# Optimization experiments

Hardware: AMD Instinct MI355X
Metric: run time of the kernel (lower is better)

Reference implementation:

```python
import jax, jax.numpy as jnp
import numpy as np

CARD = [3049, 10, 7, 3]
EMB = 16
HID = 64
COV = 10
B = 4096
S = 512
IN_DIM = 1 + COV + len(CARD) * EMB + 1  # 76


def setup_inputs() -> dict:
    key = jax.random.key(0)
    ks = jax.random.split(key, 12)
    target = jax.random.uniform(ks[0], (B, S), dtype=jnp.float32) * 100.0
    covariates = jax.random.normal(ks[1], (B, S, COV), dtype=jnp.float32)
    static_cats = jax.random.randint(ks[2], (B, len(CARD)), 0, 3)
    scale = jax.random.uniform(ks[3], (B, 1), dtype=jnp.float32) * 10.0 + 0.1
    emb0 = jax.random.normal(ks[4], (CARD[0], EMB), dtype=jnp.float32) * 0.1
    emb1 = jax.random.normal(ks[5], (CARD[1], EMB), dtype=jnp.float32) * 0.1
    emb2 = jax.random.normal(ks[6], (CARD[2], EMB), dtype=jnp.float32) * 0.1
    emb3 = jax.random.normal(ks[7], (CARD[3], EMB), dtype=jnp.float32) * 0.1
    w_ih = jax.random.normal(ks[8], (IN_DIM, 4 * HID), dtype=jnp.float32) / np.sqrt(IN_DIM)
    w_hh = jax.random.normal(ks[9], (HID, 4 * HID), dtype=jnp.float32) / np.sqrt(HID)
    bias = jnp.zeros((4 * HID,), dtype=jnp.float32)
    w_out = jax.random.normal(ks[10], (HID, 2), dtype=jnp.float32) / np.sqrt(HID)
    b_out = jnp.zeros((2,), dtype=jnp.float32)
    return dict(target=target, covariates=covariates, static_cats=static_cats,
                scale=scale, emb0=emb0, emb1=emb1, emb2=emb2, emb3=emb3,
                w_ih=w_ih, w_hh=w_hh, bias=bias, w_out=w_out, b_out=b_out)


def reference(target, covariates, static_cats, scale,
              emb0, emb1, emb2, emb3, w_ih, w_hh, bias, w_out, b_out):
    # static embedding concat: [B, 4*EMB]
    static_emb = jnp.concatenate([emb0[static_cats[:, 0]], emb1[static_cats[:, 1]],
                                  emb2[static_cats[:, 2]], emb3[static_cats[:, 3]]], axis=-1)
    log_scale = jnp.log1p(scale)                              # [B, 1]
    static_x = jnp.concatenate([static_emb, log_scale], -1)  # [B, 4*EMB+1]
    # teacher-forced previous scaled target: shifted target/scale, zero at t=0
    ps = target / jnp.maximum(scale, 1e-4)                    # [B, S]
    prev = jnp.concatenate([jnp.zeros_like(ps[:, :1]), ps[:, :-1]], axis=1)

    h0 = jnp.zeros((target.shape[0], w_hh.shape[0]), dtype=target.dtype)

    def step(carry, xs):
        h, c = carry
        p_t, cov_t = xs  # [B], [B, COV]
        x = jnp.concatenate([p_t[:, None], cov_t, static_x], axis=-1)  # [B, IN_DIM]
        gates = x @ w_ih + h @ w_hh + bias
        i, f, g, o = jnp.split(gates, 4, axis=-1)
        i = jax.nn.sigmoid(i)
        f = jax.nn.sigmoid(f)
        g = jnp.tanh(g)
        o = jax.nn.sigmoid(o)
        c = f * c + i * g
        h = o * jnp.tanh(c)
        raw = h @ w_out + b_out                    # [B, 2]
        mu_s = jax.nn.softplus(raw[:, 0]) + 1e-4   # [B]
        al = jax.nn.softplus(raw[:, 1]) + 1e-4     # [B]
        return (h, c), (mu_s, al)

    xs = (prev.T, jnp.swapaxes(covariates, 0, 1))  # time-major
    _, (mu_s, al) = jax.lax.scan(step, (h0, h0), xs)
    mus = mu_s.T * scale   # [B, S]
    alphas = al.T          # [B, S]
    return mus, alphas
```

## Files before the change

### kernel.cpp

```cpp
#include <hip/hip_runtime.h>

#define BB 4096
#define SS 512
#define NG 256
#define BT 16
#define NT 512
#define CH 32
#define HSTR 68
#define PSTR 16
#define SBSTR 264
#define OSTR 33

typedef __bf16 bf16_t;
typedef bf16_t bf16x8 __attribute__((ext_vector_type(8)));
typedef float  f32x4  __attribute__((ext_vector_type(4)));

__device__ __forceinline__ unsigned short f2bf(float x) {
    union { float f; unsigned u; } q{x};
    unsigned r = (q.u + 0x7fffu + ((q.u >> 16) & 1u)) >> 16;
    return (unsigned short)r;
}
__device__ __forceinline__ float bf2f(unsigned short s) {
    union { unsigned u; float f; } q{((unsigned)s) << 16};
    return q.f;
}
#define LOG2E 1.4426950408889634f
__device__ __forceinline__ float frcp_(float x)  { return __builtin_amdgcn_rcpf(x); }
__device__ __forceinline__ float fexp2_(float x) { return __builtin_amdgcn_exp2f(x); }
__device__ __forceinline__ float flog2_(float x) { return __builtin_amdgcn_logf(x); }
__device__ __forceinline__ float softplus_(float x){ return x > 20.0f ? x : 0.6931471805599453f * flog2_(1.0f + fexp2_(LOG2E * x)); }

__global__ __launch_bounds__(NT)
void deepar_kernel(const float* __restrict__ target, const float* __restrict__ cov,
                   const int* __restrict__ cats, const float* __restrict__ scale,
                   const float* __restrict__ emb0, const float* __restrict__ emb1,
                   const float* __restrict__ emb2, const float* __restrict__ emb3,
                   const float* __restrict__ w_ih, const float* __restrict__ w_hh,
                   const float* __restrict__ bias, const float* __restrict__ w_out,
                   const float* __restrict__ b_out, float* __restrict__ out)
{
    __shared__ __attribute__((aligned(16))) unsigned char smemA[2 * CH * BT * PSTR * 2];
    __shared__ __attribute__((aligned(16))) unsigned short hbuf[2][BT][HSTR];
    __shared__ float obuf[2][CH][OSTR];
    __shared__ float inv_s[BT], scl_s[BT];

    unsigned short* pcx   = (unsigned short*)smemA;
    float*          sbias = (float*)smemA;
    float*          sx    = (float*)(smemA + BT * SBSTR * 4);

    const int tid  = threadIdx.x;
    const int b0   = blockIdx.x * BT;
    const int lane = tid & 63;
    const int wv   = tid >> 6;
    const int qd   = lane >> 4;
    const int ln   = lane & 15;
    const int wvg  = wv & 3;
    const int tid2 = tid & 255;

    for (int i = tid; i < 2 * BT * HSTR; i += NT) ((unsigned short*)hbuf)[i] = 0;
    if (tid < BT) {
        float s = scale[b0 + tid];
        scl_s[tid] = s;
        inv_s[tid] = 1.0f / fmaxf(s, 1e-4f);
        sx[tid * 68 + 64] = log1pf(s);
    }
    if (tid < BT * 4) {
        int r = tid >> 2, e = tid & 3;
        int c = cats[(b0 + r) * 4 + e];
        const float* eb = (e == 0 ? emb0 : e == 1 ? emb1 : e == 2 ? emb2 : emb3);
        for (int j = 0; j < 16; ++j) sx[r * 68 + e * 16 + j] = eb[c * 16 + j];
    }
    __syncthreads();

    {
        const int n = tid & 255, half = tid >> 8;
        float bj = bias[n];
        float acc[8];
        #pragma unroll
        for (int r = 0; r < 8; ++r) acc[r] = bj;
        for (int k = 0; k < 65; ++k) {
            float w = w_ih[(11 + k) * NG + n];
            #pragma unroll
            for (int r = 0; r < 8; ++r) acc[r] += sx[(half * 8 + r) * 68 + k] * w;
        }
        #pragma unroll
        for (int r = 0; r < 8; ++r) sbias[(half * 8 + r) * SBSTR + n] = acc[r];
    }
    __syncthreads();

    bf16x8 bfrag[4][3];
    f32x4  sbf[4];
    {
        #pragma unroll
        for (int ti = 0; ti < 4; ++ti) {
            const float gsc = (ti == 2) ? (-2.0f * LOG2E) : (-LOG2E);
            const int n = ln + 16 * (wvg + 4 * ti);
            #pragma unroll
            for (int c = 0; c < 3; ++c) {
                #pragma unroll
                for (int j = 0; j < 8; ++j) {
                    int k = qd * 8 + 32 * c + j;
                    float w;
                    if (k < 64)                  w = w_hh[k * NG + n];
                    else if (k == 64 || k == 75) w = w_ih[n];
                    else if (k <= 74)            w = w_ih[(k - 64) * NG + n];
                    else                         w = 0.0f;
                    bfrag[ti][c][j] = (bf16_t)(w * gsc);
                }
            }
            #pragma unroll
            for (int r = 0; r < 4; ++r)
                sbf[ti][r] = sbias[(qd * 4 + r) * SBSTR + n] * gsc;
        }
    }

    bf16x8 wob0, wob1;
    f32x4  bC;
    float  scl4[4];
    #pragma unroll
    for (int j = 0; j < 8; ++j) {
        wob0[j] = (bf16_t)((ln < 2) ? w_out[(qd * 8 + j) * 2 + ln] : 0.0f);
        wob1[j] = (bf16_t)((ln < 2) ? w_out[(32 + qd * 8 + j) * 2 + ln] : 0.0f);
    }
    #pragma unroll
    for (int r = 0; r < 4; ++r) {
        bC[r]   = (ln < 2) ? b_out[ln] : 0.0f;
        scl4[r] = (ln == 0) ? scl_s[qd * 4 + r] : 1.0f;
    }

    __syncthreads();

    for (int i = tid; i < (2 * CH * BT * PSTR) / 2; i += NT) ((int*)smemA)[i] = 0;
    __syncthreads();

    if (tid < 256) {
        const int row = tid >> 4, i5 = tid & 15;
        const float* cr = cov + (size_t)(b0 + row) * (SS * 10);
        #pragma unroll
        for (int j = 0; j < 20; ++j) {
            int e = i5 + 16 * j, tp = e / 10, k = e - 10 * tp;
            pcx[((0 * CH + tp) * BT + row) * PSTR + 1 + k] = f2bf(cr[e]);
        }
        float pv0 = (i5 == 0) ? 0.0f : target[(size_t)(b0 + row) * SS + i5 - 1] * inv_s[row];
        float pv1 = target[(size_t)(b0 + row) * SS + i5 + 15] * inv_s[row];
        unsigned short m0 = f2bf(pv0), m1 = f2bf(pv1);
        pcx[((0 * CH + i5) * BT + row) * PSTR + 0]       = m0;
        pcx[((0 * CH + i5) * BT + row) * PSTR + 11]      = f2bf(pv0 - bf2f(m0));
        pcx[((0 * CH + i5 + 16) * BT + row) * PSTR + 0]  = m1;
        pcx[((0 * CH + i5 + 16) * BT + row) * PSTR + 11] = f2bf(pv1 - bf2f(m1));
    }
    __syncthreads();

    bf16x8 a2 = {};
    f32x4 acc_pre[4];
    {
        if (qd < 2)
            a2 = *(const bf16x8*)&pcx[((0 * CH + 0) * BT + ln) * PSTR + qd * 8];
        #pragma unroll
        for (int ti = 0; ti < 4; ++ti)
            acc_pre[ti] = __builtin_amdgcn_mfma_f32_16x16x32_bf16(a2, bfrag[ti][2], sbf[ti], 0, 0, 0);
    }

    float cst[2] = {0.0f, 0.0f};
    float crg[20];
    #pragma unroll
    for (int j = 0; j < 20; ++j) crg[j] = 0.0f;
    float trg0 = 0.0f, trg1 = 0.0f;

#define CELL(CI, RI)                                                            \
    {                                                                           \
        float si = frcp_(1.0f + fexp2_(acc0[RI]));                              \
        float sf = frcp_(1.0f + fexp2_(acc1[RI]));                              \
        float tg = 2.0f * frcp_(1.0f + fexp2_(acc2[RI])) - 1.0f;                \
        float so = frcp_(1.0f + fexp2_(acc3[RI]));                              \
        float cc = sf * cst[CI] + si * tg;                                      \
        cst[CI] = cc;                                                           \
        float th = 2.0f * frcp_(1.0f + fexp2_((-2.0f * LOG2E) * cc)) - 1.0f;    \
        *(bf16_t*)&hbuf[nxt][qd * 4 + RI][u] = (bf16_t)(so * th);               \
    }

    for (int t = 0; t < SS; ++t) {
        const int cur = t & 1, nxt = cur ^ 1;
        __syncthreads();

        const unsigned short* hb = &hbuf[cur][ln][0];
        bf16x8 a0 = *(const bf16x8*)(hb + qd * 8);
        bf16x8 a1 = *(const bf16x8*)(hb + 32 + qd * 8);

        f32x4 acc0 = __builtin_amdgcn_mfma_f32_16x16x32_bf16(a0, bfrag[0][0], acc_pre[0], 0, 0, 0);
        f32x4 acc1 = __builtin_amdgcn_mfma_f32_16x16x32_bf16(a0, bfrag[1][0], acc_pre[1], 0, 0, 0);
        f32x4 acc2 = __builtin_amdgcn_mfma_f32_16x16x32_bf16(a0, bfrag[2][0], acc_pre[2], 0, 0, 0);
        f32x4 acc3 = __builtin_amdgcn_mfma_f32_16x16x32_bf16(a0, bfrag[3][0], acc_pre[3], 0, 0, 0);
        acc0 = __builtin_amdgcn_mfma_f32_16x16x32_bf16(a1, bfrag[0][1], acc0, 0, 0, 0);
        acc1 = __builtin_amdgcn_mfma_f32_16x16x32_bf16(a1, bfrag[1][1], acc1, 0, 0, 0);
        acc2 = __builtin_amdgcn_mfma_f32_16x16x32_bf16(a1, bfrag[2][1], acc2, 0, 0, 0);
        acc3 = __builtin_amdgcn_mfma_f32_16x16x32_bf16(a1, bfrag[3][1], acc3, 0, 0, 0);

        if (t + 1 < SS && qd < 2)
            a2 = *(const bf16x8*)&pcx[((((t + 1) >> 5) & 1) * CH + ((t + 1) & 31)) * BT * PSTR
                                      + ln * PSTR + qd * 8];

        const int u = 16 * wvg + ln;
        if (wv < 4) { CELL(0, 0); CELL(1, 1); }
        else        { CELL(0, 2); CELL(1, 3); }

        if (t > 0 && wv == (t & 7)) {
            f32x4 hacc = __builtin_amdgcn_mfma_f32_16x16x32_bf16(a0, wob0, bC, 0, 0, 0);
            hacc = __builtin_amdgcn_mfma_f32_16x16x32_bf16(a1, wob1, hacc, 0, 0, 0);
            if (ln < 2) {
                #pragma unroll
                for (int r = 0; r < 4; ++r) {
                    float sp = softplus_(hacc[r]) + 1e-4f;
                    obuf[((t - 1) >> 5) & 1][(t - 1) & 31][ln * 16 + qd * 4 + r] = sp * scl4[r];
                }
            }
        }

        if (t + 1 < SS) {
            #pragma unroll
            for (int ti = 0; ti < 4; ++ti)
                acc_pre[ti] = __builtin_amdgcn_mfma_f32_16x16x32_bf16(a2, bfrag[ti][2], sbf[ti], 0, 0, 0);
        }

        if (wv >= 4) {
            if ((t & 31) == 0 && t < 480) {
                const int row = tid2 >> 4, i5 = tid2 & 15, t0n = t + CH;
                const float* cr = cov + (size_t)(b0 + row) * (SS * 10) + t0n * 10;
                #pragma unroll
                for (int j = 0; j < 20; ++j) crg[j] = cr[i5 + 16 * j];
                const float* tr = target + (size_t)(b0 + row) * SS + t0n + i5;
                trg0 = tr[-1];
                trg1 = tr[15];
            }

            if ((t & 31) == 16) {
                const int c = t >> 5;
                if (c < 15) {
                    const int row = tid2 >> 4, i5 = tid2 & 15, nb = (c + 1) & 1;
                    float pv0 = trg0 * inv_s[row];
                    float pv1 = trg1 * inv_s[row];
                    unsigned short m0 = f2bf(pv0), m1 = f2bf(pv1);
                    pcx[((nb * CH + i5) * BT + row) * PSTR + 0]       = m0;
                    pcx[((nb * CH + i5) * BT + row) * PSTR + 11]      = f2bf(pv0 - bf2f(m0));
                    pcx[((nb * CH + i5 + 16) * BT + row) * PSTR + 0]  = m1;
                    pcx[((nb * CH + i5 + 16) * BT + row) * PSTR + 11] = f2bf(pv1 - bf2f(m1));
                    #pragma unroll
                    for (int j = 0; j < 20; ++j) {
                        int e = i5 + 16 * j, tp = e / 10, k = e - 10 * tp;
                        pcx[((nb * CH + tp) * BT + row) * PSTR + 1 + k] = f2bf(crg[j]);
                    }
                }
                if (c >= 1) {
                    const int pb = (c - 1) & 1, t0p = (c - 1) << 5;
                    #pragma unroll
                    for (int h = 0; h < 4; ++h) {
                        int e = tid2 + 256 * h;
                        int tte = e & 31, rowe = (e >> 5) & 15, pe = e >> 9;
                        out[(pe ? (BB * SS) : 0) + (size_t)(b0 + rowe) * SS + t0p + tte] =
                            obuf[pb][tte][pe * 16 + rowe];
                    }
                }
            }
        }
    }

    __syncthreads();
    if (wv == 4) {
        const unsigned short* hb = &hbuf[0][ln][0];
        bf16x8 a0 = *(const bf16x8*)(hb + qd * 8);
        bf16x8 a1 = *(const bf16x8*)(hb + 32 + qd * 8);
        f32x4 hacc = __builtin_amdgcn_mfma_f32_16x16x32_bf16(a0, wob0, bC, 0, 0, 0);
        hacc = __builtin_amdgcn_mfma_f32_16x16x32_bf16(a1, wob1, hacc, 0, 0, 0);
        if (ln < 2) {
            #pragma unroll
            for (int r = 0; r < 4; ++r) {
                float sp = softplus_(hacc[r]) + 1e-4f;
                obuf[1][31][ln * 16 + qd * 4 + r] = sp * scl4[r];
            }
        }
    }
    __syncthreads();
    #pragma unroll
    for (int h = 0; h < 2; ++h) {
        int e = tid + NT * h;
        int tte = e & 31, rowe = (e >> 5) & 15, pe = e >> 9;
        out[(pe ? (BB * SS) : 0) + (size_t)(b0 + rowe) * SS + 480 + tte] =
            obuf[1][tte][pe * 16 + rowe];
    }
}

extern "C" void kernel_launch(void* const* d_in, const int* in_sizes, int n_in,
                              void* d_out, int out_size, void* d_ws, size_t ws_size,
                              hipStream_t stream) {
    deepar_kernel<<<BB / BT, NT, 0, stream>>>(
        (const float*)d_in[0], (const float*)d_in[1], (const int*)d_in[2],
        (const float*)d_in[3], (const float*)d_in[4], (const float*)d_in[5],
        (const float*)d_in[6], (const float*)d_in[7], (const float*)d_in[8],
        (const float*)d_in[9], (const float*)d_in[10], (const float*)d_in[11],
        (const float*)d_in[12], (float*)d_out);
}
```

Measured before the change: 592.7 us.

## Halve batch tile per block to 8 rows with 4 waves and cross-lane gate redistribution

Each block now processes 8 batch rows with 256 threads (4 waves) instead of 16 rows with 512 threads, doubling the grid to 512 blocks and adding a min-blocks-per-CU launch bound. The MFMA 16x16 tile is padded with a zero row buffer, and gate accumulators for rows 0-7 are redistributed across lanes via xor-32 shuffles so every lane computes two cell updates. The goal is more blocks to fill the CUs and cheaper per-step barriers on the serial recurrence. The cost is that half of each MFMA's rows are wasted on padding and extra shuffles are added to every time step.

```diff
diff --git a/kernel.cpp b/kernel.cpp
--- a/kernel.cpp
+++ b/kernel.cpp
@@ -3,13 +3,13 @@
 #define BB 4096
 #define SS 512
 #define NG 256
-#define BT 16
-#define NT 512
+#define BTL 8
+#define NT 256
 #define CH 32
 #define HSTR 68
 #define PSTR 16
 #define SBSTR 264
-#define OSTR 33
+#define OSTR 17
 
 typedef __bf16 bf16_t;
 typedef bf16_t bf16x8 __attribute__((ext_vector_type(8)));
@@ -30,7 +30,7 @@
 __device__ __forceinline__ float flog2_(float x) { return __builtin_amdgcn_logf(x); }
 __device__ __forceinline__ float softplus_(float x){ return x > 20.0f ? x : 0.6931471805599453f * flog2_(1.0f + fexp2_(LOG2E * x)); }
 
-__global__ __launch_bounds__(NT)
+__global__ __launch_bounds__(NT, 3)
 void deepar_kernel(const float* __restrict__ target, const float* __restrict__ cov,
                    const int* __restrict__ cats, const float* __restrict__ scale,
                    const float* __restrict__ emb0, const float* __restrict__ emb1,
@@ -39,32 +39,32 @@
                    const float* __restrict__ bias, const float* __restrict__ w_out,
                    const float* __restrict__ b_out, float* __restrict__ out)
 {
-    __shared__ __attribute__((aligned(16))) unsigned char smemA[2 * CH * BT * PSTR * 2];
-    __shared__ __attribute__((aligned(16))) unsigned short hbuf[2][BT][HSTR];
+    __shared__ __attribute__((aligned(16))) unsigned char smemA[2 * CH * BTL * PSTR * 2];
+    __shared__ __attribute__((aligned(16))) unsigned short hbuf[2][BTL][HSTR];
     __shared__ float obuf[2][CH][OSTR];
-    __shared__ float inv_s[BT], scl_s[BT];
+    __shared__ __attribute__((aligned(16))) unsigned short zb[64];
+    __shared__ float inv_s[BTL], scl_s[BTL];
 
     unsigned short* pcx   = (unsigned short*)smemA;
     float*          sbias = (float*)smemA;
-    float*          sx    = (float*)(smemA + BT * SBSTR * 4);
+    float*          sx    = (float*)(smemA + BTL * SBSTR * 4);
 
     const int tid  = threadIdx.x;
-    const int b0   = blockIdx.x * BT;
+    const int b0   = blockIdx.x * BTL;
     const int lane = tid & 63;
     const int wv   = tid >> 6;
     const int qd   = lane >> 4;
     const int ln   = lane & 15;
-    const int wvg  = wv & 3;
-    const int tid2 = tid & 255;
-
-    for (int i = tid; i < 2 * BT * HSTR; i += NT) ((unsigned short*)hbuf)[i] = 0;
-    if (tid < BT) {
+
+    for (int i = tid; i < 2 * BTL * HSTR; i += NT) ((unsigned short*)hbuf)[i] = 0;
+    if (tid < 64) zb[tid] = 0;
+    if (tid < BTL) {
         float s = scale[b0 + tid];
         scl_s[tid] = s;
         inv_s[tid] = 1.0f / fmaxf(s, 1e-4f);
         sx[tid * 68 + 64] = log1pf(s);
     }
-    if (tid < BT * 4) {
+    if (tid < BTL * 4) {
         int r = tid >> 2, e = tid & 3;
         int c = cats[(b0 + r) * 4 + e];
         const float* eb = (e == 0 ? emb0 : e == 1 ? emb1 : e == 2 ? emb2 : emb3);
@@ -73,18 +73,18 @@
     __syncthreads();
 
     {
-        const int n = tid & 255, half = tid >> 8;
+        const int n = tid;
         float bj = bias[n];
-        float acc[8];
-        #pragma unroll
-        for (int r = 0; r < 8; ++r) acc[r] = bj;
+        float acc[BTL];
+        #pragma unroll
+        for (int r = 0; r < BTL; ++r) acc[r] = bj;
         for (int k = 0; k < 65; ++k) {
             float w = w_ih[(11 + k) * NG + n];
             #pragma unroll
-            for (int r = 0; r < 8; ++r) acc[r] += sx[(half * 8 + r) * 68 + k] * w;
-        }
-        #pragma unroll
-        for (int r = 0; r < 8; ++r) sbias[(half * 8 + r) * SBSTR + n] = acc[r];
+            for (int r = 0; r < BTL; ++r) acc[r] += sx[r * 68 + k] * w;
+        }
+        #pragma unroll
+        for (int r = 0; r < BTL; ++r) sbias[r * SBSTR + n] = acc[r];
     }
     __syncthreads();
 
@@ -94,7 +94,7 @@
         #pragma unroll
         for (int ti = 0; ti < 4; ++ti) {
             const float gsc = (ti == 2) ? (-2.0f * LOG2E) : (-LOG2E);
-            const int n = ln + 16 * (wvg + 4 * ti);
+            const int n = ln + 16 * (wv + 4 * ti);
             #pragma unroll
             for (int c = 0; c < 3; ++c) {
                 #pragma unroll
@@ -110,7 +110,7 @@
             }
             #pragma unroll
             for (int r = 0; r < 4; ++r)
-                sbf[ti][r] = sbias[(qd * 4 + r) * SBSTR + n] * gsc;
+                sbf[ti][r] = sbias[((qd * 4 + r) & 7) * SBSTR + n] * gsc;
         }
     }
 
@@ -125,29 +125,26 @@
     #pragma unroll
     for (int r = 0; r < 4; ++r) {
         bC[r]   = (ln < 2) ? b_out[ln] : 0.0f;
-        scl4[r] = (ln == 0) ? scl_s[qd * 4 + r] : 1.0f;
-    }
-
-    __syncthreads();
-
-    for (int i = tid; i < (2 * CH * BT * PSTR) / 2; i += NT) ((int*)smemA)[i] = 0;
-    __syncthreads();
-
-    if (tid < 256) {
-        const int row = tid >> 4, i5 = tid & 15;
+        scl4[r] = (ln == 0) ? scl_s[(qd * 4 + r) & 7] : 1.0f;
+    }
+
+    __syncthreads();
+
+    for (int i = tid; i < (2 * CH * BTL * PSTR) / 2; i += NT) ((int*)smemA)[i] = 0;
+    __syncthreads();
+
+    {
+        const int row = tid >> 5, sl = tid & 31;
         const float* cr = cov + (size_t)(b0 + row) * (SS * 10);
         #pragma unroll
-        for (int j = 0; j < 20; ++j) {
-            int e = i5 + 16 * j, tp = e / 10, k = e - 10 * tp;
-            pcx[((0 * CH + tp) * BT + row) * PSTR + 1 + k] = f2bf(cr[e]);
-        }
-        float pv0 = (i5 == 0) ? 0.0f : target[(size_t)(b0 + row) * SS + i5 - 1] * inv_s[row];
-        float pv1 = target[(size_t)(b0 + row) * SS + i5 + 15] * inv_s[row];
-        unsigned short m0 = f2bf(pv0), m1 = f2bf(pv1);
-        pcx[((0 * CH + i5) * BT + row) * PSTR + 0]       = m0;
-        pcx[((0 * CH + i5) * BT + row) * PSTR + 11]      = f2bf(pv0 - bf2f(m0));
-        pcx[((0 * CH + i5 + 16) * BT + row) * PSTR + 0]  = m1;
-        pcx[((0 * CH + i5 + 16) * BT + row) * PSTR + 11] = f2bf(pv1 - bf2f(m1));
+        for (int j = 0; j < 10; ++j) {
+            int e = sl + 32 * j, tp = e / 10, k = e - 10 * tp;
+            pcx[((0 * CH + tp) * BTL + row) * PSTR + 1 + k] = f2bf(cr[e]);
+        }
+        float pv = (sl == 0) ? 0.0f : target[(size_t)(b0 + row) * SS + sl - 1] * inv_s[row];
+        unsigned short m0 = f2bf(pv);
+        pcx[((0 * CH + sl) * BTL + row) * PSTR + 0]  = m0;
+        pcx[((0 * CH + sl) * BTL + row) * PSTR + 11] = f2bf(pv - bf2f(m0));
     }
     __syncthreads();
 
@@ -155,35 +152,25 @@
     f32x4 acc_pre[4];
     {
         if (qd < 2)
-            a2 = *(const bf16x8*)&pcx[((0 * CH + 0) * BT + ln) * PSTR + qd * 8];
+            a2 = *(const bf16x8*)((ln < BTL)
+                    ? &pcx[((0 * CH + 0) * BTL + ln) * PSTR + qd * 8]
+                    : &zb[qd * 8]);
         #pragma unroll
         for (int ti = 0; ti < 4; ++ti)
             acc_pre[ti] = __builtin_amdgcn_mfma_f32_16x16x32_bf16(a2, bfrag[ti][2], sbf[ti], 0, 0, 0);
     }
 
     float cst[2] = {0.0f, 0.0f};
-    float crg[20];
+    float crg[10];
     #pragma unroll
-    for (int j = 0; j < 20; ++j) crg[j] = 0.0f;
-    float trg0 = 0.0f, trg1 = 0.0f;
-
-#define CELL(CI, RI)                                                            \
-    {                                                                           \
-        float si = frcp_(1.0f + fexp2_(acc0[RI]));                              \
-        float sf = frcp_(1.0f + fexp2_(acc1[RI]));                              \
-        float tg = 2.0f * frcp_(1.0f + fexp2_(acc2[RI])) - 1.0f;                \
-        float so = frcp_(1.0f + fexp2_(acc3[RI]));                              \
-        float cc = sf * cst[CI] + si * tg;                                      \
-        cst[CI] = cc;                                                           \
-        float th = 2.0f * frcp_(1.0f + fexp2_((-2.0f * LOG2E) * cc)) - 1.0f;    \
-        *(bf16_t*)&hbuf[nxt][qd * 4 + RI][u] = (bf16_t)(so * th);               \
-    }
+    for (int j = 0; j < 10; ++j) crg[j] = 0.0f;
+    float trgv = 0.0f;
 
     for (int t = 0; t < SS; ++t) {
         const int cur = t & 1, nxt = cur ^ 1;
         __syncthreads();
 
-        const unsigned short* hb = &hbuf[cur][ln][0];
+        const unsigned short* hb = (ln < BTL) ? &hbuf[cur][ln][0] : &zb[0];
         bf16x8 a0 = *(const bf16x8*)(hb + qd * 8);
         bf16x8 a1 = *(const bf16x8*)(hb + 32 + qd * 8);
 
@@ -197,21 +184,43 @@
         acc3 = __builtin_amdgcn_mfma_f32_16x16x32_bf16(a1, bfrag[3][1], acc3, 0, 0, 0);
 
         if (t + 1 < SS && qd < 2)
-            a2 = *(const bf16x8*)&pcx[((((t + 1) >> 5) & 1) * CH + ((t + 1) & 31)) * BT * PSTR
-                                      + ln * PSTR + qd * 8];
-
-        const int u = 16 * wvg + ln;
-        if (wv < 4) { CELL(0, 0); CELL(1, 1); }
-        else        { CELL(0, 2); CELL(1, 3); }
-
-        if (t > 0 && wv == (t & 7)) {
+            a2 = *(const bf16x8*)((ln < BTL)
+                    ? &pcx[((((t + 1) >> 5) & 1) * CH + ((t + 1) & 31)) * BTL * PSTR
+                           + ln * PSTR + qd * 8]
+                    : &zb[qd * 8]);
+
+        float xi0 = __shfl_xor(acc0[2], 32), xi1 = __shfl_xor(acc0[3], 32);
+        float xf0 = __shfl_xor(acc1[2], 32), xf1 = __shfl_xor(acc1[3], 32);
+        float xg0 = __shfl_xor(acc2[2], 32), xg1 = __shfl_xor(acc2[3], 32);
+        float xo0 = __shfl_xor(acc3[2], 32), xo1 = __shfl_xor(acc3[3], 32);
+        const bool hi = (qd >= 2);
+        float gi[2] = { hi ? xi0 : acc0[0], hi ? xi1 : acc0[1] };
+        float gf[2] = { hi ? xf0 : acc1[0], hi ? xf1 : acc1[1] };
+        float gg[2] = { hi ? xg0 : acc2[0], hi ? xg1 : acc2[1] };
+        float go[2] = { hi ? xo0 : acc3[0], hi ? xo1 : acc3[1] };
+
+        const int rowb = (qd & 1) * 4 + (qd >> 1) * 2;
+        const int u = 16 * wv + ln;
+        #pragma unroll
+        for (int rr = 0; rr < 2; ++rr) {
+            float si = frcp_(1.0f + fexp2_(gi[rr]));
+            float sf = frcp_(1.0f + fexp2_(gf[rr]));
+            float tg = 2.0f * frcp_(1.0f + fexp2_(gg[rr])) - 1.0f;
+            float so = frcp_(1.0f + fexp2_(go[rr]));
+            float cc = sf * cst[rr] + si * tg;
+            cst[rr] = cc;
+            float th = 2.0f * frcp_(1.0f + fexp2_((-2.0f * LOG2E) * cc)) - 1.0f;
+            *(bf16_t*)&hbuf[nxt][rowb + rr][u] = (bf16_t)(so * th);
+        }
+
+        if (t > 0 && wv == (t & 3)) {
             f32x4 hacc = __builtin_amdgcn_mfma_f32_16x16x32_bf16(a0, wob0, bC, 0, 0, 0);
             hacc = __builtin_amdgcn_mfma_f32_16x16x32_bf16(a1, wob1, hacc, 0, 0, 0);
-            if (ln < 2) {
+            if (ln < 2 && qd < 2) {
                 #pragma unroll
                 for (int r = 0; r < 4; ++r) {
                     float sp = softplus_(hacc[r]) + 1e-4f;
-                    obuf[((t - 1) >> 5) & 1][(t - 1) & 31][ln * 16 + qd * 4 + r] = sp * scl4[r];
+                    obuf[((t - 1) >> 5) & 1][(t - 1) & 31][(qd * 4 + r) * 2 + ln] = sp * scl4[r];
                 }
             }
         }
@@ -222,60 +231,53 @@
                 acc_pre[ti] = __builtin_amdgcn_mfma_f32_16x16x32_bf16(a2, bfrag[ti][2], sbf[ti], 0, 0, 0);
         }
 
-        if (wv >= 4) {
-            if ((t & 31) == 0 && t < 480) {
-                const int row = tid2 >> 4, i5 = tid2 & 15, t0n = t + CH;
-                const float* cr = cov + (size_t)(b0 + row) * (SS * 10) + t0n * 10;
+        if ((t & 31) == 0 && t < 480) {
+            const int row = tid >> 5, sl = tid & 31, t0n = t + CH;
+            const float* cr = cov + (size_t)(b0 + row) * (SS * 10) + t0n * 10;
+            #pragma unroll
+            for (int j = 0; j < 10; ++j) crg[j] = cr[sl + 32 * j];
+            trgv = target[(size_t)(b0 + row) * SS + t0n + sl - 1];
+        }
+
+        if ((t & 31) == 16) {
+            const int c = t >> 5;
+            if (c < 15) {
+                const int row = tid >> 5, sl = tid & 31, nb = (c + 1) & 1;
+                float pv = trgv * inv_s[row];
+                unsigned short m0 = f2bf(pv);
+                pcx[((nb * CH + sl) * BTL + row) * PSTR + 0]  = m0;
+                pcx[((nb * CH + sl) * BTL + row) * PSTR + 11] = f2bf(pv - bf2f(m0));
                 #pragma unroll
-                for (int j = 0; j < 20; ++j) crg[j] = cr[i5 + 16 * j];
-                const float* tr = target + (size_t)(b0 + row) * SS + t0n + i5;
-                trg0 = tr[-1];
-                trg1 = tr[15];
-            }
-
-            if ((t & 31) == 16) {
-                const int c = t >> 5;
-                if (c < 15) {
-                    const int row = tid2 >> 4, i5 = tid2 & 15, nb = (c + 1) & 1;
-                    float pv0 = trg0 * inv_s[row];
-                    float pv1 = trg1 * inv_s[row];
-                    unsigned short m0 = f2bf(pv0), m1 = f2bf(pv1);
-                    pcx[((nb * CH + i5) * BT + row) * PSTR + 0]       = m0;
-                    pcx[((nb * CH + i5) * BT + row) * PSTR + 11]      = f2bf(pv0 - bf2f(m0));
-                    pcx[((nb * CH + i5 + 16) * BT + row) * PSTR + 0]  = m1;
-                    pcx[((nb * CH + i5 + 16) * BT + row) * PSTR + 11] = f2bf(pv1 - bf2f(m1));
-                    #pragma unroll
-                    for (int j = 0; j < 20; ++j) {
-                        int e = i5 + 16 * j, tp = e / 10, k = e - 10 * tp;
-                        pcx[((nb * CH + tp) * BT + row) * PSTR + 1 + k] = f2bf(crg[j]);
-                    }
+                for (int j = 0; j < 10; ++j) {
+                    int e = sl + 32 * j, tp = e / 10, k = e - 10 * tp;
+                    pcx[((nb * CH + tp) * BTL + row) * PSTR + 1 + k] = f2bf(crg[j]);
                 }
-                if (c >= 1) {
-                    const int pb = (c - 1) & 1, t0p = (c - 1) << 5;
-                    #pragma unroll
-                    for (int h = 0; h < 4; ++h) {
-                        int e = tid2 + 256 * h;
-                        int tte = e & 31, rowe = (e >> 5) & 15, pe = e >> 9;
-                        out[(pe ? (BB * SS) : 0) + (size_t)(b0 + rowe) * SS + t0p + tte] =
-                            obuf[pb][tte][pe * 16 + rowe];
-                    }
+            }
+            if (c >= 1) {
+                const int pb = (c - 1) & 1, t0p = (c - 1) << 5;
+                #pragma unroll
+                for (int h = 0; h < 2; ++h) {
+                    int e = tid + NT * h;
+                    int tte = e & 31, rowe = (e >> 5) & 7, pe = e >> 8;
+                    out[(pe ? (BB * SS) : 0) + (size_t)(b0 + rowe) * SS + t0p + tte] =
+                        obuf[pb][tte][rowe * 2 + pe];
                 }
             }
         }
     }
 
     __syncthreads();
-    if (wv == 4) {
-        const unsigned short* hb = &hbuf[0][ln][0];
+    if (wv == 0) {
+        const unsigned short* hb = (ln < BTL) ? &hbuf[0][ln][0] : &zb[0];
         bf16x8 a0 = *(const bf16x8*)(hb + qd * 8);
         bf16x8 a1 = *(const bf16x8*)(hb + 32 + qd * 8);
         f32x4 hacc = __builtin_amdgcn_mfma_f32_16x16x32_bf16(a0, wob0, bC, 0, 0, 0);
         hacc = __builtin_amdgcn_mfma_f32_16x16x32_bf16(a1, wob1, hacc, 0, 0, 0);
-        if (ln < 2) {
+        if (ln < 2 && qd < 2) {
             #pragma unroll
             for (int r = 0; r < 4; ++r) {
                 float sp = softplus_(hacc[r]) + 1e-4f;
-                obuf[1][31][ln * 16 + qd * 4 + r] = sp * scl4[r];
+                obuf[1][31][(qd * 4 + r) * 2 + ln] = sp * scl4[r];
             }
         }
     }
@@ -283,16 +285,16 @@
     #pragma unroll
     for (int h = 0; h < 2; ++h) {
         int e = tid + NT * h;
-        int tte = e & 31, rowe = (e >> 5) & 15, pe = e >> 9;
+        int tte = e & 31, rowe = (e >> 5) & 7, pe = e >> 8;
         out[(pe ? (BB * SS) : 0) + (size_t)(b0 + rowe) * SS + 480 + tte] =
-            obuf[1][tte][pe * 16 + rowe];
+            obuf[1][tte][rowe * 2 + pe];
     }
 }
 
 extern "C" void kernel_launch(void* const* d_in, const int* in_sizes, int n_in,
                               void* d_out, int out_size, void* d_ws, size_t ws_size,
                               hipStream_t stream) {
-    deepar_kernel<<<BB / BT, NT, 0, stream>>>(
+    deepar_kernel<<<BB / BTL, NT, 0, stream>>>(
         (const float*)d_in[0], (const float*)d_in[1], (const int*)d_in[2],
         (const float*)d_in[3], (const float*)d_in[4], (const float*)d_in[5],
         (const float*)d_in[6], (const float*)d_in[7], (const float*)d_in[8],
```

Result: slower. 721.4 us (+21.7%).
